# Kernel optimization log

Measured on AMD Instinct MI355X. Metric: run time of the kernel, lower is better.

## Reference

```python
import jax, jax.numpy as jnp
import numpy as np


def setup_inputs() -> dict:
    key = jax.random.key(0)
    k1, k2, k3 = jax.random.split(key, 3)
    m, h, t, d = 4, 16, 1024, 64
    s = 128  # max_relative_distance
    return {
        "attnQ": jax.random.normal(k1, (m, h, t, d), dtype=jnp.float32),
        "attnK": jax.random.normal(k2, (m, h, t, d), dtype=jnp.float32),
        "pe": jax.random.normal(k3, (2 * s + 1, d), dtype=jnp.float32),
        "max_relative_distance": s,
    }


def reference(attnQ, attnK, pe, max_relative_distance):
    # attnQ: [m, h, t1, d], attnK: [m, h, t2, d] (only t2 is used), pe: [2s+1, d]
    t1 = attnQ.shape[-2]
    t2 = attnK.shape[-2]
    s = max_relative_distance
    # clipped relative distances, shifted into table index range [0, 2s]
    rel = jnp.arange(t1)[:, None] - jnp.arange(t2)[None, :]          # [t1, t2]
    rel = jnp.clip(rel, -s, s) + min(s + 1, max(t1, t2)) - 1         # [t1, t2]
    emb = pe[rel]                                                    # [t1, t2, d]
    emb = jnp.transpose(emb, (0, 2, 1))                              # [t1, d, t2]
    # per-query-position matmul of Q rows against relative embeddings
    return jnp.einsum('mhtd,tds->mhts', attnQ, emb)                  # [m, h, t1, t2]
```

## Files before the change

### kernel.cpp

```cpp
#include <hip/hip_runtime.h>
#include <stdint.h>
#include <stddef.h>

#define T_LEN 1024
#define D_DIM 64
#define NPE   257
#define BI    16
#define QP_ST 266

typedef _Float16 h16;
typedef h16   h16x8 __attribute__((ext_vector_type(8)));
typedef float f32x4 __attribute__((ext_vector_type(4)));

__device__ __forceinline__ unsigned short f2h_bits(float f) {
    union { h16 h; unsigned short u; } c; c.h = (h16)f; return c.u;
}
__device__ __forceinline__ float lo_h(uint32_t p) {
    union { uint32_t u; h16 h[2]; } c; c.u = p; return (float)c.h[0];
}
__device__ __forceinline__ float hi_h(uint32_t p) {
    union { uint32_t u; h16 h[2]; } c; c.u = p; return (float)c.h[1];
}
__device__ __forceinline__ float4 ld4(const float* p) {
    return *reinterpret_cast<const float4*>(p);
}
__device__ __forceinline__ h16x8 cvt8h(float4 a, float4 b) {
    h16x8 r;
    r[0] = (h16)a.x; r[1] = (h16)a.y; r[2] = (h16)a.z; r[3] = (h16)a.w;
    r[4] = (h16)b.x; r[5] = (h16)b.y; r[6] = (h16)b.z; r[7] = (h16)b.w;
    return r;
}

#define SPLIT1(hi, lo, idx, val)                      \
    { const float _v = (val); const h16 _h = (h16)_v; \
      hi[idx] = _h; lo[idx] = (h16)(_v - (float)_h); }

__global__ __launch_bounds__(256, 2)
void relpos_fused(const float* __restrict__ Q,
                  const float* __restrict__ pe,
                  float* __restrict__ out) {
    __shared__ unsigned short qp_s[BI][QP_ST];

    const int tid   = threadIdx.x;
    const int mh    = blockIdx.x;
    const int i0    = blockIdx.y * BI;
    const int wave  = tid >> 6;
    const int lane  = tid & 63;
    const int row16 = lane & 15;
    const int kgrp  = lane >> 4;

    const float* qrow = Q + ((size_t)mh * T_LEN + i0 + row16) * D_DIM + kgrp * 8;
    const float4 qa = ld4(qrow);
    const float4 qb = ld4(qrow + 4);
    const float4 qc = ld4(qrow + 32);
    const float4 qd = ld4(qrow + 36);

    h16x8 a0h, a0l, a1h, a1l;
    SPLIT1(a0h, a0l, 0, qa.x) SPLIT1(a0h, a0l, 1, qa.y)
    SPLIT1(a0h, a0l, 2, qa.z) SPLIT1(a0h, a0l, 3, qa.w)
    SPLIT1(a0h, a0l, 4, qb.x) SPLIT1(a0h, a0l, 5, qb.y)
    SPLIT1(a0h, a0l, 6, qb.z) SPLIT1(a0h, a0l, 7, qb.w)
    SPLIT1(a1h, a1l, 0, qc.x) SPLIT1(a1h, a1l, 1, qc.y)
    SPLIT1(a1h, a1l, 2, qc.z) SPLIT1(a1h, a1l, 3, qc.w)
    SPLIT1(a1h, a1l, 4, qd.x) SPLIT1(a1h, a1l, 5, qd.y)
    SPLIT1(a1h, a1l, 6, qd.z) SPLIT1(a1h, a1l, 7, qd.w)

#pragma unroll
    for (int n = 0; n < 4; ++n) {
        const int cb = (wave * 4 + n) * 16;
        const float* prow = pe + (size_t)(cb + row16) * D_DIM + kgrp * 8;
        const h16x8 b0 = cvt8h(ld4(prow),      ld4(prow + 4));
        const h16x8 b1 = cvt8h(ld4(prow + 32), ld4(prow + 36));
        f32x4 acc = {0.f, 0.f, 0.f, 0.f};
        acc = __builtin_amdgcn_mfma_f32_16x16x32_f16(a0h, b0, acc, 0, 0, 0);
        acc = __builtin_amdgcn_mfma_f32_16x16x32_f16(a1h, b1, acc, 0, 0, 0);
        acc = __builtin_amdgcn_mfma_f32_16x16x32_f16(a0l, b0, acc, 0, 0, 0);
        acc = __builtin_amdgcn_mfma_f32_16x16x32_f16(a1l, b1, acc, 0, 0, 0);
#pragma unroll
        for (int j = 0; j < 4; ++j)
            qp_s[kgrp * 4 + j][4 + cb + row16] = f2h_bits(acc[j]);
        if (cb == 0 && row16 == 0) {
#pragma unroll
            for (int j = 0; j < 4; ++j) {
                const unsigned short v = f2h_bits(acc[j]);
                unsigned short* qr = &qp_s[kgrp * 4 + j][0];
                qr[0] = v; qr[1] = v; qr[2] = v; qr[3] = v;
            }
        }
    }
    if (wave == 3) {
        const float* prow = pe + (size_t)256 * D_DIM + kgrp * 8;
        const h16x8 b0 = cvt8h(ld4(prow),      ld4(prow + 4));
        const h16x8 b1 = cvt8h(ld4(prow + 32), ld4(prow + 36));
        f32x4 acc = {0.f, 0.f, 0.f, 0.f};
        acc = __builtin_amdgcn_mfma_f32_16x16x32_f16(a0h, b0, acc, 0, 0, 0);
        acc = __builtin_amdgcn_mfma_f32_16x16x32_f16(a1h, b1, acc, 0, 0, 0);
        acc = __builtin_amdgcn_mfma_f32_16x16x32_f16(a0l, b0, acc, 0, 0, 0);
        acc = __builtin_amdgcn_mfma_f32_16x16x32_f16(a1l, b1, acc, 0, 0, 0);
        if (row16 == 0) {
#pragma unroll
            for (int j = 0; j < 4; ++j) {
                const unsigned short v = f2h_bits(acc[j]);
                unsigned short* qr = &qp_s[kgrp * 4 + j][0];
                qr[260] = v; qr[261] = v; qr[262] = v; qr[263] = v; qr[264] = v;
            }
        }
    }
    __syncthreads();

    const int j0 = tid << 2;
    float4* dst = reinterpret_cast<float4*>(
                      out + ((size_t)mh * T_LEN + i0) * T_LEN) + tid;

#pragma unroll 4
    for (int r = 0; r < BI; ++r) {
        const int i = i0 + r;
        int cb = i - j0 + 125;
        cb = cb < -4 ? -4 : (cb > 257 ? 257 : cb);
        const int s = cb + 4;
        const uint32_t* row = reinterpret_cast<const uint32_t*>(&qp_s[r][0]);
        const int d0 = s >> 1;
        const uint32_t w0 = row[d0], w1 = row[d0 + 1], w2 = row[d0 + 2];
        const uint32_t sh = (uint32_t)(s & 1) << 4;
        const uint32_t p01 = __builtin_amdgcn_alignbit(w1, w0, sh);
        const uint32_t p23 = __builtin_amdgcn_alignbit(w2, w1, sh);
        float4 v;
        v.x = hi_h(p23);
        v.y = lo_h(p23);
        v.z = hi_h(p01);
        v.w = lo_h(p01);
        *dst = v;
        dst += T_LEN / 4;
    }
}

extern "C" void kernel_launch(void* const* d_in, const int* in_sizes, int n_in,
                              void* d_out, int out_size, void* d_ws, size_t ws_size,
                              hipStream_t stream) {
    const float* Q  = (const float*)d_in[0];
    const float* pe = (const float*)d_in[2];
    float* out = (float*)d_out;

    const int mh = in_sizes[0] / (T_LEN * D_DIM);
    dim3 grid(mh, T_LEN / BI);
    relpos_fused<<<grid, 256, 0, stream>>>(Q, pe, out);
}
```

Before: 73.22 us.

## Make blocks persistent over several row tiles with double-buffered LDS and register-held pe

```diff
diff --git a/kernel.cpp b/kernel.cpp
--- a/kernel.cpp
+++ b/kernel.cpp
@@ -7,6 +7,7 @@
 #define NPE   257
 #define BI    16
 #define QP_ST 266
+#define NT    8
 
 typedef _Float16 h16;
 typedef h16   h16x8 __attribute__((ext_vector_type(8)));
@@ -39,98 +40,136 @@
 void relpos_fused(const float* __restrict__ Q,
                   const float* __restrict__ pe,
                   float* __restrict__ out) {
-    __shared__ unsigned short qp_s[BI][QP_ST];
+    __shared__ unsigned short qp_s[2][BI][QP_ST];
 
     const int tid   = threadIdx.x;
     const int mh    = blockIdx.x;
-    const int i0    = blockIdx.y * BI;
+    const int by    = blockIdx.y;
     const int wave  = tid >> 6;
     const int lane  = tid & 63;
     const int row16 = lane & 15;
     const int kgrp  = lane >> 4;
 
-    const float* qrow = Q + ((size_t)mh * T_LEN + i0 + row16) * D_DIM + kgrp * 8;
-    const float4 qa = ld4(qrow);
-    const float4 qb = ld4(qrow + 4);
-    const float4 qc = ld4(qrow + 32);
-    const float4 qd = ld4(qrow + 36);
+#define PE_LOAD(N, B0, B1)                                                     \
+    h16x8 B0, B1;                                                              \
+    {                                                                          \
+        const float* prow = pe + (size_t)(wave * 64 + (N) * 16 + row16) * D_DIM \
+                               + kgrp * 8;                                     \
+        B0 = cvt8h(ld4(prow),      ld4(prow + 4));                             \
+        B1 = cvt8h(ld4(prow + 32), ld4(prow + 36));                            \
+    }
+    PE_LOAD(0, pb0_0, pb1_0)
+    PE_LOAD(1, pb0_1, pb1_1)
+    PE_LOAD(2, pb0_2, pb1_2)
+    PE_LOAD(3, pb0_3, pb1_3)
+    h16x8 pb0_t16, pb1_t16;
+    if (wave == 3) {
+        const float* prow = pe + (size_t)256 * D_DIM + kgrp * 8;
+        pb0_t16 = cvt8h(ld4(prow),      ld4(prow + 4));
+        pb1_t16 = cvt8h(ld4(prow + 32), ld4(prow + 36));
+    }
 
-    h16x8 a0h, a0l, a1h, a1l;
-    SPLIT1(a0h, a0l, 0, qa.x) SPLIT1(a0h, a0l, 1, qa.y)
-    SPLIT1(a0h, a0l, 2, qa.z) SPLIT1(a0h, a0l, 3, qa.w)
-    SPLIT1(a0h, a0l, 4, qb.x) SPLIT1(a0h, a0l, 5, qb.y)
-    SPLIT1(a0h, a0l, 6, qb.z) SPLIT1(a0h, a0l, 7, qb.w)
-    SPLIT1(a1h, a1l, 0, qc.x) SPLIT1(a1h, a1l, 1, qc.y)
-    SPLIT1(a1h, a1l, 2, qc.z) SPLIT1(a1h, a1l, 3, qc.w)
-    SPLIT1(a1h, a1l, 4, qd.x) SPLIT1(a1h, a1l, 5, qd.y)
-    SPLIT1(a1h, a1l, 6, qd.z) SPLIT1(a1h, a1l, 7, qd.w)
+    float4 nqa, nqb, nqc, nqd;
+#define QLOAD(IT)                                                              \
+    {                                                                          \
+        const float* qrow = Q + ((size_t)mh * T_LEN + (IT) * BI + row16) * D_DIM \
+                              + kgrp * 8;                                      \
+        nqa = ld4(qrow);      nqb = ld4(qrow + 4);                             \
+        nqc = ld4(qrow + 32); nqd = ld4(qrow + 36);                            \
+    }
 
+#define TILE(N, B0, B1, BUF)                                                   \
+    {                                                                          \
+        f32x4 acc = {0.f, 0.f, 0.f, 0.f};                                      \
+        acc = __builtin_amdgcn_mfma_f32_16x16x32_f16(a0h, B0, acc, 0, 0, 0);   \
+        acc = __builtin_amdgcn_mfma_f32_16x16x32_f16(a1h, B1, acc, 0, 0, 0);   \
+        acc = __builtin_amdgcn_mfma_f32_16x16x32_f16(a0l, B0, acc, 0, 0, 0);   \
+        acc = __builtin_amdgcn_mfma_f32_16x16x32_f16(a1l, B1, acc, 0, 0, 0);   \
+        const int cb = wave * 64 + (N) * 16;                                   \
+        qp_s[BUF][kgrp * 4 + 0][4 + cb + row16] = f2h_bits(acc[0]);            \
+        qp_s[BUF][kgrp * 4 + 1][4 + cb + row16] = f2h_bits(acc[1]);            \
+        qp_s[BUF][kgrp * 4 + 2][4 + cb + row16] = f2h_bits(acc[2]);            \
+        qp_s[BUF][kgrp * 4 + 3][4 + cb + row16] = f2h_bits(acc[3]);            \
+        if ((N) == 0 && wave == 0 && row16 == 0) {                             \
+            _Pragma("unroll")                                                  \
+            for (int j = 0; j < 4; ++j) {                                      \
+                const unsigned short v = f2h_bits(acc[j]);                     \
+                unsigned short* qr = &qp_s[BUF][kgrp * 4 + j][0];              \
+                qr[0] = v; qr[1] = v; qr[2] = v; qr[3] = v;                    \
+            }                                                                  \
+        }                                                                      \
+    }
+
+#define BCOMPUTE(BUF)                                                          \
+    {                                                                          \
+        h16x8 a0h, a0l, a1h, a1l;                                             \
+        SPLIT1(a0h, a0l, 0, nqa.x) SPLIT1(a0h, a0l, 1, nqa.y)                 \
+        SPLIT1(a0h, a0l, 2, nqa.z) SPLIT1(a0h, a0l, 3, nqa.w)                 \
+        SPLIT1(a0h, a0l, 4, nqb.x) SPLIT1(a0h, a0l, 5, nqb.y)                 \
+        SPLIT1(a0h, a0l, 6, nqb.z) SPLIT1(a0h, a0l, 7, nqb.w)                 \
+        SPLIT1(a1h, a1l, 0, nqc.x) SPLIT1(a1h, a1l, 1, nqc.y)                 \
+        SPLIT1(a1h, a1l, 2, nqc.z) SPLIT1(a1h, a1l, 3, nqc.w)                 \
+        SPLIT1(a1h, a1l, 4, nqd.x) SPLIT1(a1h, a1l, 5, nqd.y)                 \
+        SPLIT1(a1h, a1l, 6, nqd.z) SPLIT1(a1h, a1l, 7, nqd.w)                 \
+        TILE(0, pb0_0, pb1_0, BUF)                                             \
+        TILE(1, pb0_1, pb1_1, BUF)                                             \
+        TILE(2, pb0_2, pb1_2, BUF)                                             \
+        TILE(3, pb0_3, pb1_3, BUF)                                             \
+        if (wave == 3) {                \
+            f32x4 acc = {0.f, 0.f, 0.f, 0.f};                                  \
+            acc = __builtin_amdgcn_mfma_f32_16x16x32_f16(a0h, pb0_t16, acc, 0, 0, 0); \
+            acc = __builtin_amdgcn_mfma_f32_16x16x32_f16(a1h, pb1_t16, acc, 0, 0, 0); \
+            acc = __builtin_amdgcn_mfma_f32_16x16x32_f16(a0l, pb0_t16, acc, 0, 0, 0); \
+            acc = __builtin_amdgcn_mfma_f32_16x16x32_f16(a1l, pb1_t16, acc, 0, 0, 0); \
+            if (row16 == 0) {                                                  \
+                _Pragma("unroll")                                              \
+                for (int j = 0; j < 4; ++j) {                                  \
+                    const unsigned short v = f2h_bits(acc[j]);                 \
+                    unsigned short* qr = &qp_s[BUF][kgrp * 4 + j][0];          \
+                    qr[260] = v; qr[261] = v; qr[262] = v;                     \
+                    qr[263] = v; qr[264] = v;                                  \
+                }                                                              \
+            }                                                                  \
+        }                                                                      \
+    }
+
+    QLOAD(by * NT)
+    BCOMPUTE(0)
+
+    const int j0 = tid << 2;
 #pragma unroll
-    for (int n = 0; n < 4; ++n) {
-        const int cb = (wave * 4 + n) * 16;
-        const float* prow = pe + (size_t)(cb + row16) * D_DIM + kgrp * 8;
-        const h16x8 b0 = cvt8h(ld4(prow),      ld4(prow + 4));
-        const h16x8 b1 = cvt8h(ld4(prow + 32), ld4(prow + 36));
-        f32x4 acc = {0.f, 0.f, 0.f, 0.f};
-        acc = __builtin_amdgcn_mfma_f32_16x16x32_f16(a0h, b0, acc, 0, 0, 0);
-        acc = __builtin_amdgcn_mfma_f32_16x16x32_f16(a1h, b1, acc, 0, 0, 0);
-        acc = __builtin_amdgcn_mfma_f32_16x16x32_f16(a0l, b0, acc, 0, 0, 0);
-        acc = __builtin_amdgcn_mfma_f32_16x16x32_f16(a1l, b1, acc, 0, 0, 0);
-#pragma unroll
-        for (int j = 0; j < 4; ++j)
-            qp_s[kgrp * 4 + j][4 + cb + row16] = f2h_bits(acc[j]);
-        if (cb == 0 && row16 == 0) {
-#pragma unroll
-            for (int j = 0; j < 4; ++j) {
-                const unsigned short v = f2h_bits(acc[j]);
-                unsigned short* qr = &qp_s[kgrp * 4 + j][0];
-                qr[0] = v; qr[1] = v; qr[2] = v; qr[3] = v;
+    for (int t = 0; t < NT; ++t) {
+        __syncthreads();
+        if (t + 1 < NT) { QLOAD(by * NT + t + 1) }
+
+        {
+            const int it = by * NT + t;
+            float4* dst = reinterpret_cast<float4*>(
+                              out + ((size_t)mh * T_LEN + it * BI) * T_LEN) + tid;
+#pragma unroll 4
+            for (int r = 0; r < BI; ++r) {
+                const int i = it * BI + r;
+                int cbs = i - j0 + 125;
+                cbs = cbs < -4 ? -4 : (cbs > 257 ? 257 : cbs);
+                const int s = cbs + 4;
+                const uint32_t* row =
+                    reinterpret_cast<const uint32_t*>(&qp_s[t & 1][r][0]);
+                const int d0 = s >> 1;
+                const uint32_t w0 = row[d0], w1 = row[d0 + 1], w2 = row[d0 + 2];
+                const uint32_t sh = (uint32_t)(s & 1) << 4;
+                const uint32_t p01 = __builtin_amdgcn_alignbit(w1, w0, sh);
+                const uint32_t p23 = __builtin_amdgcn_alignbit(w2, w1, sh);
+                float4 v;
+                v.x = hi_h(p23);
+                v.y = lo_h(p23);
+                v.z = hi_h(p01);
+                v.w = lo_h(p01);
+                *dst = v;
+                dst += T_LEN / 4;
             }
         }
-    }
-    if (wave == 3) {
-        const float* prow = pe + (size_t)256 * D_DIM + kgrp * 8;
-        const h16x8 b0 = cvt8h(ld4(prow),      ld4(prow + 4));
-        const h16x8 b1 = cvt8h(ld4(prow + 32), ld4(prow + 36));
-        f32x4 acc = {0.f, 0.f, 0.f, 0.f};
-        acc = __builtin_amdgcn_mfma_f32_16x16x32_f16(a0h, b0, acc, 0, 0, 0);
-        acc = __builtin_amdgcn_mfma_f32_16x16x32_f16(a1h, b1, acc, 0, 0, 0);
-        acc = __builtin_amdgcn_mfma_f32_16x16x32_f16(a0l, b0, acc, 0, 0, 0);
-        acc = __builtin_amdgcn_mfma_f32_16x16x32_f16(a1l, b1, acc, 0, 0, 0);
-        if (row16 == 0) {
-#pragma unroll
-            for (int j = 0; j < 4; ++j) {
-                const unsigned short v = f2h_bits(acc[j]);
-                unsigned short* qr = &qp_s[kgrp * 4 + j][0];
-                qr[260] = v; qr[261] = v; qr[262] = v; qr[263] = v; qr[264] = v;
-            }
-        }
-    }
-    __syncthreads();
 
-    const int j0 = tid << 2;
-    float4* dst = reinterpret_cast<float4*>(
-                      out + ((size_t)mh * T_LEN + i0) * T_LEN) + tid;
-
-#pragma unroll 4
-    for (int r = 0; r < BI; ++r) {
-        const int i = i0 + r;
-        int cb = i - j0 + 125;
-        cb = cb < -4 ? -4 : (cb > 257 ? 257 : cb);
-        const int s = cb + 4;
-        const uint32_t* row = reinterpret_cast<const uint32_t*>(&qp_s[r][0]);
-        const int d0 = s >> 1;
-        const uint32_t w0 = row[d0], w1 = row[d0 + 1], w2 = row[d0 + 2];
-        const uint32_t sh = (uint32_t)(s & 1) << 4;
-        const uint32_t p01 = __builtin_amdgcn_alignbit(w1, w0, sh);
-        const uint32_t p23 = __builtin_amdgcn_alignbit(w2, w1, sh);
-        float4 v;
-        v.x = hi_h(p23);
-        v.y = lo_h(p23);
-        v.z = hi_h(p01);
-        v.w = lo_h(p01);
-        *dst = v;
-        dst += T_LEN / 4;
+        if (t + 1 < NT) { BCOMPUTE((t + 1) & 1) }
     }
 }
 
@@ -142,6 +181,6 @@
     float* out = (float*)d_out;
 
     const int mh = in_sizes[0] / (T_LEN * D_DIM);
-    dim3 grid(mh, T_LEN / BI);
+    dim3 grid(mh, (T_LEN / BI) / NT);
     relpos_fused<<<grid, 256, 0, stream>>>(Q, pe, out);
 }
```

Measured after the change: 60.92 us. 1.2x faster.

## Stage pe fragments in LDS once per block and compute per-wave row tiles

Applied to the files above, without the earlier changes.

```diff
diff --git a/kernel.cpp b/kernel.cpp
--- a/kernel.cpp
+++ b/kernel.cpp
@@ -4,13 +4,15 @@
 
 #define T_LEN 1024
 #define D_DIM 64
-#define NPE   257
-#define BI    16
-#define QP_ST 266
+#define NFRAG 18
+#define S_SH  292
+#define WROWS 16
 
 typedef _Float16 h16;
 typedef h16   h16x8 __attribute__((ext_vector_type(8)));
 typedef float f32x4 __attribute__((ext_vector_type(4)));
+
+union frag_cast { uint4 u; h16x8 h; };
 
 __device__ __forceinline__ unsigned short f2h_bits(float f) {
     union { h16 h; unsigned short u; } c; c.h = (h16)f; return c.u;
@@ -39,98 +41,96 @@
 void relpos_fused(const float* __restrict__ Q,
                   const float* __restrict__ pe,
                   float* __restrict__ out) {
-    __shared__ unsigned short qp_s[BI][QP_ST];
+    __shared__ uint4 pe_frag[NFRAG][2][64];
+    __shared__ unsigned short sc[4][WROWS][S_SH];
 
     const int tid   = threadIdx.x;
     const int mh    = blockIdx.x;
-    const int i0    = blockIdx.y * BI;
+    const int bg    = blockIdx.y;
     const int wave  = tid >> 6;
     const int lane  = tid & 63;
     const int row16 = lane & 15;
     const int kgrp  = lane >> 4;
 
-    const float* qrow = Q + ((size_t)mh * T_LEN + i0 + row16) * D_DIM + kgrp * 8;
-    const float4 qa = ld4(qrow);
-    const float4 qb = ld4(qrow + 4);
-    const float4 qc = ld4(qrow + 32);
-    const float4 qd = ld4(qrow + 36);
-
-    h16x8 a0h, a0l, a1h, a1l;
-    SPLIT1(a0h, a0l, 0, qa.x) SPLIT1(a0h, a0l, 1, qa.y)
-    SPLIT1(a0h, a0l, 2, qa.z) SPLIT1(a0h, a0l, 3, qa.w)
-    SPLIT1(a0h, a0l, 4, qb.x) SPLIT1(a0h, a0l, 5, qb.y)
-    SPLIT1(a0h, a0l, 6, qb.z) SPLIT1(a0h, a0l, 7, qb.w)
-    SPLIT1(a1h, a1l, 0, qc.x) SPLIT1(a1h, a1l, 1, qc.y)
-    SPLIT1(a1h, a1l, 2, qc.z) SPLIT1(a1h, a1l, 3, qc.w)
-    SPLIT1(a1h, a1l, 4, qd.x) SPLIT1(a1h, a1l, 5, qd.y)
-    SPLIT1(a1h, a1l, 6, qd.z) SPLIT1(a1h, a1l, 7, qd.w)
-
-#pragma unroll
-    for (int n = 0; n < 4; ++n) {
-        const int cb = (wave * 4 + n) * 16;
-        const float* prow = pe + (size_t)(cb + row16) * D_DIM + kgrp * 8;
-        const h16x8 b0 = cvt8h(ld4(prow),      ld4(prow + 4));
-        const h16x8 b1 = cvt8h(ld4(prow + 32), ld4(prow + 36));
-        f32x4 acc = {0.f, 0.f, 0.f, 0.f};
-        acc = __builtin_amdgcn_mfma_f32_16x16x32_f16(a0h, b0, acc, 0, 0, 0);
-        acc = __builtin_amdgcn_mfma_f32_16x16x32_f16(a1h, b1, acc, 0, 0, 0);
-        acc = __builtin_amdgcn_mfma_f32_16x16x32_f16(a0l, b0, acc, 0, 0, 0);
-        acc = __builtin_amdgcn_mfma_f32_16x16x32_f16(a1l, b1, acc, 0, 0, 0);
-#pragma unroll
-        for (int j = 0; j < 4; ++j)
-            qp_s[kgrp * 4 + j][4 + cb + row16] = f2h_bits(acc[j]);
-        if (cb == 0 && row16 == 0) {
-#pragma unroll
-            for (int j = 0; j < 4; ++j) {
-                const unsigned short v = f2h_bits(acc[j]);
-                unsigned short* qr = &qp_s[kgrp * 4 + j][0];
-                qr[0] = v; qr[1] = v; qr[2] = v; qr[3] = v;
-            }
-        }
-    }
-    if (wave == 3) {
-        const float* prow = pe + (size_t)256 * D_DIM + kgrp * 8;
-        const h16x8 b0 = cvt8h(ld4(prow),      ld4(prow + 4));
-        const h16x8 b1 = cvt8h(ld4(prow + 32), ld4(prow + 36));
-        f32x4 acc = {0.f, 0.f, 0.f, 0.f};
-        acc = __builtin_amdgcn_mfma_f32_16x16x32_f16(a0h, b0, acc, 0, 0, 0);
-        acc = __builtin_amdgcn_mfma_f32_16x16x32_f16(a1h, b1, acc, 0, 0, 0);
-        acc = __builtin_amdgcn_mfma_f32_16x16x32_f16(a0l, b0, acc, 0, 0, 0);
-        acc = __builtin_amdgcn_mfma_f32_16x16x32_f16(a1l, b1, acc, 0, 0, 0);
-        if (row16 == 0) {
-#pragma unroll
-            for (int j = 0; j < 4; ++j) {
-                const unsigned short v = f2h_bits(acc[j]);
-                unsigned short* qr = &qp_s[kgrp * 4 + j][0];
-                qr[260] = v; qr[261] = v; qr[262] = v; qr[263] = v; qr[264] = v;
-            }
-        }
+    for (int f = tid; f < NFRAG * 64; f += 256) {
+        const int n   = f >> 6;
+        const int l   = f & 63;
+        const int r16 = l & 15;
+        const int kg  = l >> 4;
+        int row = n * 16 + r16;
+        row = row > 256 ? 256 : row;
+        if (n == 17) row = 0;
+        const float* prow = pe + (size_t)row * D_DIM + kg * 8;
+        frag_cast b0, b1;
+        b0.h = cvt8h(ld4(prow),      ld4(prow + 4));
+        b1.h = cvt8h(ld4(prow + 32), ld4(prow + 36));
+        pe_frag[n][0][l] = b0.u;
+        pe_frag[n][1][l] = b1.u;
     }
     __syncthreads();
 
-    const int j0 = tid << 2;
-    float4* dst = reinterpret_cast<float4*>(
-                      out + ((size_t)mh * T_LEN + i0) * T_LEN) + tid;
+    unsigned short* const scw = &sc[wave][0][0];
 
+#pragma unroll
+    for (int p = 0; p < 2; ++p) {
+        const int i0 = bg * 128 + p * 64 + wave * 16;
+
+        const float* qrow = Q + ((size_t)mh * T_LEN + i0 + row16) * D_DIM + kgrp * 8;
+        const float4 qa = ld4(qrow);
+        const float4 qb = ld4(qrow + 4);
+        const float4 qc = ld4(qrow + 32);
+        const float4 qd = ld4(qrow + 36);
+        h16x8 a0h, a0l, a1h, a1l;
+        SPLIT1(a0h, a0l, 0, qa.x) SPLIT1(a0h, a0l, 1, qa.y)
+        SPLIT1(a0h, a0l, 2, qa.z) SPLIT1(a0h, a0l, 3, qa.w)
+        SPLIT1(a0h, a0l, 4, qb.x) SPLIT1(a0h, a0l, 5, qb.y)
+        SPLIT1(a0h, a0l, 6, qb.z) SPLIT1(a0h, a0l, 7, qb.w)
+        SPLIT1(a1h, a1l, 0, qc.x) SPLIT1(a1h, a1l, 1, qc.y)
+        SPLIT1(a1h, a1l, 2, qc.z) SPLIT1(a1h, a1l, 3, qc.w)
+        SPLIT1(a1h, a1l, 4, qd.x) SPLIT1(a1h, a1l, 5, qd.y)
+        SPLIT1(a1h, a1l, 6, qd.z) SPLIT1(a1h, a1l, 7, qd.w)
+
+#pragma unroll
+        for (int n = 0; n < NFRAG; ++n) {
+            frag_cast u0, u1;
+            u0.u = pe_frag[n][0][lane];
+            u1.u = pe_frag[n][1][lane];
+            f32x4 acc = {0.f, 0.f, 0.f, 0.f};
+            acc = __builtin_amdgcn_mfma_f32_16x16x32_f16(a0h, u0.h, acc, 0, 0, 0);
+            acc = __builtin_amdgcn_mfma_f32_16x16x32_f16(a1h, u1.h, acc, 0, 0, 0);
+            acc = __builtin_amdgcn_mfma_f32_16x16x32_f16(a0l, u0.h, acc, 0, 0, 0);
+            acc = __builtin_amdgcn_mfma_f32_16x16x32_f16(a1l, u1.h, acc, 0, 0, 0);
+            const int c = (n < 17) ? n * 16 + row16 : row16 - 16;
+#pragma unroll
+            for (int j = 0; j < 4; ++j) {
+                const int r    = kgrp * 4 + j;
+                const int tmin = (r & 7) + 8;
+                int t = tmin + 256 - c;
+                if (n == 16) t = (t < 0) ? 288 : t;
+                scw[r * S_SH + t] = f2h_bits(acc[j]);
+            }
+        }
+
+        float* const outb = out + ((size_t)mh * T_LEN + i0) * T_LEN;
 #pragma unroll 4
-    for (int r = 0; r < BI; ++r) {
-        const int i = i0 + r;
-        int cb = i - j0 + 125;
-        cb = cb < -4 ? -4 : (cb > 257 ? 257 : cb);
-        const int s = cb + 4;
-        const uint32_t* row = reinterpret_cast<const uint32_t*>(&qp_s[r][0]);
-        const int d0 = s >> 1;
-        const uint32_t w0 = row[d0], w1 = row[d0 + 1], w2 = row[d0 + 2];
-        const uint32_t sh = (uint32_t)(s & 1) << 4;
-        const uint32_t p01 = __builtin_amdgcn_alignbit(w1, w0, sh);
-        const uint32_t p23 = __builtin_amdgcn_alignbit(w2, w1, sh);
-        float4 v;
-        v.x = hi_h(p23);
-        v.y = lo_h(p23);
-        v.z = hi_h(p01);
-        v.w = lo_h(p01);
-        *dst = v;
-        dst += T_LEN / 4;
+        for (int r = 0; r < WROWS; ++r) {
+            const int i    = i0 + r;
+            const int tmin = (r & 7) + 8;
+            const int A    = i - 128 - tmin;
+            const unsigned short* srow = scw + r * S_SH;
+            float* drow = outb + (size_t)r * T_LEN;
+#pragma unroll
+            for (int s = 0; s < 4; ++s) {
+                const int j0 = s * 256 + lane * 4;
+                int jc = j0 < A ? A : j0;
+                jc = jc > A + 276 ? A + 276 : jc;
+                const uint2 w = *reinterpret_cast<const uint2*>(srow + (jc - A));
+                float4 v;
+                v.x = lo_h(w.x); v.y = hi_h(w.x);
+                v.z = lo_h(w.y); v.w = hi_h(w.y);
+                *reinterpret_cast<float4*>(drow + j0) = v;
+            }
+        }
     }
 }
 
@@ -142,6 +142,6 @@
     float* out = (float*)d_out;
 
     const int mh = in_sizes[0] / (T_LEN * D_DIM);
-    dim3 grid(mh, T_LEN / BI);
+    dim3 grid(mh, T_LEN / 128);
     relpos_fused<<<grid, 256, 0, stream>>>(Q, pe, out);
 }
```

Result: slower. 100.4 us (+37.2%).
